# Kernel tuning notes

Measured on AMD Instinct MI355X. Metric: run time of the kernel, lower is better.

Reference implementation:

```python
import jax, jax.numpy as jnp
import numpy as np

N = 10000
E = 160000
EMB = 10
ITERS = 3


def _linear_params(key, fan_in, fan_out):
    kw, kb = jax.random.split(key)
    # xavier-normal-ish init for the weight, small uniform for bias (as torch Linear default scale)
    w = jax.random.normal(kw, (fan_in, fan_out), dtype=jnp.float32) * np.float32(np.sqrt(2.0 / (fan_in + fan_out)))
    b = jax.random.uniform(kb, (fan_out,), dtype=jnp.float32, minval=-0.1, maxval=0.1)
    return w, b


def setup_inputs() -> dict:
    key = jax.random.key(0)
    ks = jax.random.split(key, 10)
    features = jax.random.normal(ks[0], (N,), dtype=jnp.float32)
    weights = jax.random.uniform(ks[1], (E,), dtype=jnp.float32)
    adjacency = jax.random.uniform(ks[2], (N, N), dtype=jnp.float32)
    ws_w, ws_b = _linear_params(ks[3], 1, EMB)          # w_selected
    wnp_w, wnp_b = _linear_params(ks[4], EMB, EMB)      # w_nbpriors
    wnw_w, wnw_b = _linear_params(ks[5], EMB, EMB)      # w_nbweights
    wew_w, wew_b = _linear_params(ks[6], 1, EMB)        # w_nbweights_ew
    wqr_w, wqr_b = _linear_params(ks[7], 2 * EMB, 1)    # w_q_reduc
    wqa_w, wqa_b = _linear_params(ks[8], EMB, EMB)      # w_q_allembed
    wqact_w, wqact_b = _linear_params(ks[9], EMB, EMB)  # w_q_action
    return {
        "features": features, "weights": weights, "adjacency": adjacency,
        "ws_w": ws_w, "ws_b": ws_b,
        "wnp_w": wnp_w, "wnp_b": wnp_b,
        "wnw_w": wnw_w, "wnw_b": wnw_b,
        "wew_w": wew_w, "wew_b": wew_b,
        "wqr_w": wqr_w, "wqr_b": wqr_b,
        "wqa_w": wqa_w, "wqa_b": wqa_b,
        "wqact_w": wqact_w, "wqact_b": wqact_b,
    }


def reference(features, weights, adjacency,
              ws_w, ws_b, wnp_w, wnp_b, wnw_w, wnw_b, wew_w, wew_b,
              wqr_w, wqr_b, wqa_w, wqa_b, wqact_w, wqact_b):
    n = adjacency.shape[0]
    # v_selected = w_selected(features[:, None])  -> (N, EMB)
    v_selected = features[:, None] @ ws_w + ws_b
    # edge weight embedding, summed over edges -> single (EMB,) vector
    edge_emb = jax.nn.relu(weights[:, None] @ wew_w + wew_b)  # (E, EMB)
    v_weights = jnp.sum(edge_emb, axis=0) @ wnw_w + wnw_b     # (EMB,)

    embeddings = jnp.zeros((n, EMB), dtype=features.dtype)
    for _ in range(ITERS):  # small fixed iteration count
        v_priors = (adjacency @ embeddings) @ wnp_w + wnp_b   # (N, EMB)
        embeddings = jax.nn.relu(v_selected + v_weights + v_priors)

    sumembed = jnp.sum(embeddings, axis=0) @ wqa_w + wqa_b    # (EMB,)
    peract = embeddings @ wqact_w + wqact_b                   # (N, EMB)
    q_in = jnp.concatenate([jnp.broadcast_to(sumembed[None, :], (n, EMB)), peract], axis=1)
    q_vals = (q_in @ wqr_w + wqr_b)[:, 0]                     # (N,)
    return q_vals, embeddings
```

## Files before the change

### kernel.cpp

```cpp
#include <hip/hip_runtime.h>

#define N_NODES 10000
#define EMB 10
#define NCHUNK 2500
#define ROWS 4

typedef float f32x4 __attribute__((ext_vector_type(4)));

#define WS_SEDGE 0
#define WS_CBASE 16
#define WS_SSUM  32
#define WS_QVEC  48
#define WS_EMBA  64
#define WS_EMBTA (64 + 100000)
#define WS_EMBB  (64 + 200000)
#define WS_EMBTB (64 + 300000)

__global__ void k_edge_sum(const float* __restrict__ w, int E,
                           const float* __restrict__ wew_w,
                           const float* __restrict__ wew_b,
                           float* __restrict__ sEdge) {
    __shared__ float red[4][EMB];
    float a[EMB], b[EMB], acc[EMB];
#pragma unroll
    for (int j = 0; j < EMB; ++j) { a[j] = wew_w[j]; b[j] = wew_b[j]; acc[j] = 0.f; }
    for (int e = blockIdx.x * blockDim.x + threadIdx.x; e < E; e += gridDim.x * blockDim.x) {
        float we = w[e];
#pragma unroll
        for (int j = 0; j < EMB; ++j) acc[j] += fmaxf(we * a[j] + b[j], 0.f);
    }
#pragma unroll
    for (int m = 1; m < 64; m <<= 1)
#pragma unroll
        for (int j = 0; j < EMB; ++j) acc[j] += __shfl_xor(acc[j], m, 64);
    int wave = threadIdx.x >> 6, lane = threadIdx.x & 63;
    if (lane == 0)
#pragma unroll
        for (int j = 0; j < EMB; ++j) red[wave][j] = acc[j];
    __syncthreads();
    if (threadIdx.x < EMB)
        atomicAdd(&sEdge[threadIdx.x],
                  red[0][threadIdx.x] + red[1][threadIdx.x] + red[2][threadIdx.x] + red[3][threadIdx.x]);
}

__global__ void k_prep1(const float* __restrict__ sEdge, const float* __restrict__ wnw_w,
                        const float* __restrict__ wnw_b, const float* __restrict__ ws_b,
                        float* __restrict__ cbase) {
    int j = threadIdx.x;
    if (j < EMB) {
        float v = wnw_b[j];
        for (int k = 0; k < EMB; ++k) v += sEdge[k] * wnw_w[k * EMB + j];
        cbase[j] = v + ws_b[j];
    }
}

__global__ void k_emb1(const float* __restrict__ f, const float* __restrict__ ws_w,
                       const float* __restrict__ cbase, const float* __restrict__ wnp_b,
                       float* __restrict__ emb, float* __restrict__ embT) {
    int i = blockIdx.x * blockDim.x + threadIdx.x;
    if (i < N_NODES) {
        float fi = f[i];
#pragma unroll
        for (int j = 0; j < EMB; ++j) {
            float v = fmaxf(fi * ws_w[j] + cbase[j] + wnp_b[j], 0.f);
            emb[(size_t)i * EMB + j] = v;
            embT[(size_t)j * N_NODES + i] = v;
        }
    }
}

__global__ __launch_bounds__(256) void k_iter(
    const float* __restrict__ A, const float* __restrict__ embT_in,
    const float* __restrict__ f, const float* __restrict__ ws_w,
    const float* __restrict__ cbase, const float* __restrict__ wnp_w,
    const float* __restrict__ wnp_b,
    float* __restrict__ emb_out, float* __restrict__ embT_out) {
    const int tid  = threadIdx.x;
    const int wave = tid >> 6;
    const int lane = tid & 63;
    const int r0 = blockIdx.x * ROWS;

    float acc[ROWS][EMB] = {};

    const f32x4* A0 = (const f32x4*)(A + (size_t)(r0 + 0) * N_NODES);
    const f32x4* A1 = (const f32x4*)(A + (size_t)(r0 + 1) * N_NODES);
    const f32x4* A2 = (const f32x4*)(A + (size_t)(r0 + 2) * N_NODES);
    const f32x4* A3 = (const f32x4*)(A + (size_t)(r0 + 3) * N_NODES);

#pragma unroll 1
    for (int s = 0; s < 9; ++s) {
        int c = s * 256 + tid;
        f32x4 a0 = __builtin_nontemporal_load(A0 + c);
        f32x4 a1 = __builtin_nontemporal_load(A1 + c);
        f32x4 a2 = __builtin_nontemporal_load(A2 + c);
        f32x4 a3 = __builtin_nontemporal_load(A3 + c);
#pragma unroll
        for (int j = 0; j < EMB; ++j) {
            f32x4 e = ((const f32x4*)(embT_in + (size_t)j * N_NODES))[c];
            acc[0][j] += a0.x * e.x + a0.y * e.y + a0.z * e.z + a0.w * e.w;
            acc[1][j] += a1.x * e.x + a1.y * e.y + a1.z * e.z + a1.w * e.w;
            acc[2][j] += a2.x * e.x + a2.y * e.y + a2.z * e.z + a2.w * e.w;
            acc[3][j] += a3.x * e.x + a3.y * e.y + a3.z * e.z + a3.w * e.w;
        }
    }
    if (tid < NCHUNK - 9 * 256) {
        int c = 9 * 256 + tid;
        f32x4 a0 = __builtin_nontemporal_load(A0 + c);
        f32x4 a1 = __builtin_nontemporal_load(A1 + c);
        f32x4 a2 = __builtin_nontemporal_load(A2 + c);
        f32x4 a3 = __builtin_nontemporal_load(A3 + c);
#pragma unroll
        for (int j = 0; j < EMB; ++j) {
            f32x4 e = ((const f32x4*)(embT_in + (size_t)j * N_NODES))[c];
            acc[0][j] += a0.x * e.x + a0.y * e.y + a0.z * e.z + a0.w * e.w;
            acc[1][j] += a1.x * e.x + a1.y * e.y + a1.z * e.z + a1.w * e.w;
            acc[2][j] += a2.x * e.x + a2.y * e.y + a2.z * e.z + a2.w * e.w;
            acc[3][j] += a3.x * e.x + a3.y * e.y + a3.z * e.z + a3.w * e.w;
        }
    }

#pragma unroll
    for (int m = 1; m < 64; m <<= 1)
#pragma unroll
        for (int r = 0; r < ROWS; ++r)
#pragma unroll
            for (int j = 0; j < EMB; ++j) acc[r][j] += __shfl_xor(acc[r][j], m, 64);

    __shared__ float part[4][ROWS * EMB];
    if (lane == 0)
#pragma unroll
        for (int r = 0; r < ROWS; ++r)
#pragma unroll
            for (int j = 0; j < EMB; ++j) part[wave][r * EMB + j] = acc[r][j];
    __syncthreads();

    if (tid < ROWS * EMB) {
        int r = tid / EMB, j = tid % EMB;
        float v = wnp_b[j];
#pragma unroll
        for (int k = 0; k < EMB; ++k) {
            float yk = part[0][r * EMB + k] + part[1][r * EMB + k] +
                       part[2][r * EMB + k] + part[3][r * EMB + k];
            v += yk * wnp_w[k * EMB + j];
        }
        int i = r0 + r;
        v = fmaxf(f[i] * ws_w[j] + cbase[j] + v, 0.f);
        emb_out[(size_t)i * EMB + j] = v;
        embT_out[(size_t)j * N_NODES + i] = v;
    }
}

__global__ void k_colsum(const float* __restrict__ embT, float* __restrict__ ssum) {
    int j = blockIdx.x % EMB;
    int s = blockIdx.x / EMB;
    float acc = 0.f;
    for (int i = s * blockDim.x + threadIdx.x; i < N_NODES; i += (gridDim.x / EMB) * blockDim.x)
        acc += embT[(size_t)j * N_NODES + i];
#pragma unroll
    for (int m = 1; m < 64; m <<= 1) acc += __shfl_xor(acc, m, 64);
    __shared__ float red[4];
    int wave = threadIdx.x >> 6, lane = threadIdx.x & 63;
    if (lane == 0) red[wave] = acc;
    __syncthreads();
    if (threadIdx.x == 0) atomicAdd(&ssum[j], red[0] + red[1] + red[2] + red[3]);
}

__global__ void k_prep2(const float* __restrict__ ssum, const float* __restrict__ wqa_w,
                        const float* __restrict__ wqa_b, const float* __restrict__ wqr_w,
                        const float* __restrict__ wqr_b, const float* __restrict__ wqact_w,
                        const float* __restrict__ wqact_b,
                        float* __restrict__ qvec, float* __restrict__ qc) {
    int t = threadIdx.x;
    float contrib = 0.f;
    if (t < EMB) {
        float se = wqa_b[t];
        for (int k = 0; k < EMB; ++k) se += ssum[k] * wqa_w[k * EMB + t];
        contrib = se * wqr_w[t] + wqact_b[t] * wqr_w[EMB + t];
        float qv = 0.f;
        for (int j = 0; j < EMB; ++j) qv += wqact_w[t * EMB + j] * wqr_w[EMB + j];
        qvec[t] = qv;
    }
#pragma unroll
    for (int m = 1; m < 64; m <<= 1) contrib += __shfl_xor(contrib, m, 64);
    if (t == 0) qc[0] = contrib + wqr_b[0];
}

__global__ void k_out(const float* __restrict__ emb, const float* __restrict__ qvec,
                      const float* __restrict__ qc, float* __restrict__ out) {
    int i = blockIdx.x * blockDim.x + threadIdx.x;
    if (i < N_NODES) {
        float q = qc[0];
        float row[EMB];
#pragma unroll
        for (int j = 0; j < EMB; ++j) {
            row[j] = emb[(size_t)i * EMB + j];
            q += row[j] * qvec[j];
        }
        out[i] = q;
#pragma unroll
        for (int j = 0; j < EMB; ++j) out[N_NODES + (size_t)i * EMB + j] = row[j];
    }
}

extern "C" void kernel_launch(void* const* d_in, const int* in_sizes, int n_in,
                              void* d_out, int out_size, void* d_ws, size_t ws_size,
                              hipStream_t stream) {
    (void)n_in; (void)out_size; (void)ws_size;
    const float* f      = (const float*)d_in[0];
    const float* w      = (const float*)d_in[1];
    const float* A      = (const float*)d_in[2];
    const float* ws_w   = (const float*)d_in[3];
    const float* ws_b   = (const float*)d_in[4];
    const float* wnp_w  = (const float*)d_in[5];
    const float* wnp_b  = (const float*)d_in[6];
    const float* wnw_w  = (const float*)d_in[7];
    const float* wnw_b  = (const float*)d_in[8];
    const float* wew_w  = (const float*)d_in[9];
    const float* wew_b  = (const float*)d_in[10];
    const float* wqr_w  = (const float*)d_in[11];
    const float* wqr_b  = (const float*)d_in[12];
    const float* wqa_w  = (const float*)d_in[13];
    const float* wqa_b  = (const float*)d_in[14];
    const float* wqact_w = (const float*)d_in[15];
    const float* wqact_b = (const float*)d_in[16];
    float* ws  = (float*)d_ws;
    float* out = (float*)d_out;
    const int E = in_sizes[1];

    hipMemsetAsync(ws, 0, 64 * sizeof(float), stream);
    k_edge_sum<<<256, 256, 0, stream>>>(w, E, wew_w, wew_b, ws + WS_SEDGE);
    k_prep1<<<1, 64, 0, stream>>>(ws + WS_SEDGE, wnw_w, wnw_b, ws_b, ws + WS_CBASE);
    k_emb1<<<(N_NODES + 255) / 256, 256, 0, stream>>>(f, ws_w, ws + WS_CBASE, wnp_b,
                                                      ws + WS_EMBA, ws + WS_EMBTA);
    k_iter<<<N_NODES / ROWS, 256, 0, stream>>>(A, ws + WS_EMBTA, f, ws_w, ws + WS_CBASE,
                                               wnp_w, wnp_b, ws + WS_EMBB, ws + WS_EMBTB);
    k_iter<<<N_NODES / ROWS, 256, 0, stream>>>(A, ws + WS_EMBTB, f, ws_w, ws + WS_CBASE,
                                               wnp_w, wnp_b, ws + WS_EMBA, ws + WS_EMBTA);
    k_colsum<<<80, 256, 0, stream>>>(ws + WS_EMBTA, ws + WS_SSUM);
    k_prep2<<<1, 64, 0, stream>>>(ws + WS_SSUM, wqa_w, wqa_b, wqr_w, wqr_b,
                                  wqact_w, wqact_b, ws + WS_QVEC, ws + WS_QVEC + 10);
    k_out<<<(N_NODES + 255) / 256, 256, 0, stream>>>(ws + WS_EMBA, ws + WS_QVEC,
                                                     ws + WS_QVEC + 10, out);
}
```

Before: 694.4 us.

## Fuse prep/first-embedding/colsum kernels into iteration kernels and reverse block order

```diff
diff --git a/kernel.cpp b/kernel.cpp
--- a/kernel.cpp
+++ b/kernel.cpp
@@ -8,13 +8,8 @@
 typedef float f32x4 __attribute__((ext_vector_type(4)));
 
 #define WS_SEDGE 0
-#define WS_CBASE 16
-#define WS_SSUM  32
-#define WS_QVEC  48
-#define WS_EMBA  64
-#define WS_EMBTA (64 + 100000)
-#define WS_EMBB  (64 + 200000)
-#define WS_EMBTB (64 + 300000)
+#define WS_SSUM  16
+#define WS_EMBT  64
 
 __global__ void k_edge_sum(const float* __restrict__ w, int E,
                            const float* __restrict__ wew_w,
@@ -43,42 +38,33 @@
                   red[0][threadIdx.x] + red[1][threadIdx.x] + red[2][threadIdx.x] + red[3][threadIdx.x]);
 }
 
-__global__ void k_prep1(const float* __restrict__ sEdge, const float* __restrict__ wnw_w,
-                        const float* __restrict__ wnw_b, const float* __restrict__ ws_b,
-                        float* __restrict__ cbase) {
-    int j = threadIdx.x;
-    if (j < EMB) {
-        float v = wnw_b[j];
-        for (int k = 0; k < EMB; ++k) v += sEdge[k] * wnw_w[k * EMB + j];
-        cbase[j] = v + ws_b[j];
-    }
-}
-
-__global__ void k_emb1(const float* __restrict__ f, const float* __restrict__ ws_w,
-                       const float* __restrict__ cbase, const float* __restrict__ wnp_b,
-                       float* __restrict__ emb, float* __restrict__ embT) {
-    int i = blockIdx.x * blockDim.x + threadIdx.x;
-    if (i < N_NODES) {
-        float fi = f[i];
-#pragma unroll
-        for (int j = 0; j < EMB; ++j) {
-            float v = fmaxf(fi * ws_w[j] + cbase[j] + wnp_b[j], 0.f);
-            emb[(size_t)i * EMB + j] = v;
-            embT[(size_t)j * N_NODES + i] = v;
-        }
-    }
-}
-
+template <bool FIRST>
 __global__ __launch_bounds__(256) void k_iter(
     const float* __restrict__ A, const float* __restrict__ embT_in,
     const float* __restrict__ f, const float* __restrict__ ws_w,
-    const float* __restrict__ cbase, const float* __restrict__ wnp_w,
-    const float* __restrict__ wnp_b,
-    float* __restrict__ emb_out, float* __restrict__ embT_out) {
+    const float* __restrict__ ws_b, const float* __restrict__ wnp_w,
+    const float* __restrict__ wnp_b, const float* __restrict__ wnw_w,
+    const float* __restrict__ wnw_b, const float* __restrict__ sEdge,
+    float* __restrict__ embT_out, float* __restrict__ emb_out,
+    float* __restrict__ ssum) {
     const int tid  = threadIdx.x;
     const int wave = tid >> 6;
     const int lane = tid & 63;
-    const int r0 = blockIdx.x * ROWS;
+    const int bid  = FIRST ? blockIdx.x : (gridDim.x - 1 - blockIdx.x);
+    const int r0   = bid * ROWS;
+
+    __shared__ float s_cb2[EMB];
+    if (tid < EMB) {
+        int j = tid;
+        float v = wnw_b[j];
+#pragma unroll
+        for (int k = 0; k < EMB; ++k) v += sEdge[k] * wnw_w[k * EMB + j];
+        s_cb2[j] = v + ws_b[j] + wnp_b[j];
+    }
+    __syncthreads();
+    float cb2[EMB], wsw[EMB];
+#pragma unroll
+    for (int j = 0; j < EMB; ++j) { cb2[j] = s_cb2[j]; wsw[j] = ws_w[j]; }
 
     float acc[ROWS][EMB] = {};
 
@@ -86,38 +72,43 @@
     const f32x4* A1 = (const f32x4*)(A + (size_t)(r0 + 1) * N_NODES);
     const f32x4* A2 = (const f32x4*)(A + (size_t)(r0 + 2) * N_NODES);
     const f32x4* A3 = (const f32x4*)(A + (size_t)(r0 + 3) * N_NODES);
+    const f32x4* F4 = (const f32x4*)f;
+
+#define BODY(c)                                                                     \
+    {                                                                               \
+        f32x4 a0, a1, a2, a3;                                                       \
+        if (FIRST) {                                                                \
+            a0 = A0[c]; a1 = A1[c]; a2 = A2[c]; a3 = A3[c];                         \
+        } else {                                                                    \
+            a0 = __builtin_nontemporal_load(A0 + (c));                              \
+            a1 = __builtin_nontemporal_load(A1 + (c));                              \
+            a2 = __builtin_nontemporal_load(A2 + (c));                              \
+            a3 = __builtin_nontemporal_load(A3 + (c));                              \
+        }                                                                           \
+        f32x4 f4;                                                                   \
+        if (FIRST) f4 = F4[c];                                                      \
+        _Pragma("unroll")                                                           \
+        for (int j = 0; j < EMB; ++j) {                                             \
+            f32x4 e;                                                               \
+            if (FIRST) {                                                            \
+                e.x = fmaxf(f4.x * wsw[j] + cb2[j], 0.f);                           \
+                e.y = fmaxf(f4.y * wsw[j] + cb2[j], 0.f);                           \
+                e.z = fmaxf(f4.z * wsw[j] + cb2[j], 0.f);                           \
+                e.w = fmaxf(f4.w * wsw[j] + cb2[j], 0.f);                           \
+            } else {                                                                \
+                e = ((const f32x4*)(embT_in + (size_t)j * N_NODES))[c];             \
+            }                                                                       \
+            acc[0][j] += a0.x * e.x + a0.y * e.y + a0.z * e.z + a0.w * e.w;         \
+            acc[1][j] += a1.x * e.x + a1.y * e.y + a1.z * e.z + a1.w * e.w;         \
+            acc[2][j] += a2.x * e.x + a2.y * e.y + a2.z * e.z + a2.w * e.w;         \
+            acc[3][j] += a3.x * e.x + a3.y * e.y + a3.z * e.z + a3.w * e.w;         \
+        }                                                                           \
+    }
 
 #pragma unroll 1
-    for (int s = 0; s < 9; ++s) {
-        int c = s * 256 + tid;
-        f32x4 a0 = __builtin_nontemporal_load(A0 + c);
-        f32x4 a1 = __builtin_nontemporal_load(A1 + c);
-        f32x4 a2 = __builtin_nontemporal_load(A2 + c);
-        f32x4 a3 = __builtin_nontemporal_load(A3 + c);
-#pragma unroll
-        for (int j = 0; j < EMB; ++j) {
-            f32x4 e = ((const f32x4*)(embT_in + (size_t)j * N_NODES))[c];
-            acc[0][j] += a0.x * e.x + a0.y * e.y + a0.z * e.z + a0.w * e.w;
-            acc[1][j] += a1.x * e.x + a1.y * e.y + a1.z * e.z + a1.w * e.w;
-            acc[2][j] += a2.x * e.x + a2.y * e.y + a2.z * e.z + a2.w * e.w;
-            acc[3][j] += a3.x * e.x + a3.y * e.y + a3.z * e.z + a3.w * e.w;
-        }
-    }
-    if (tid < NCHUNK - 9 * 256) {
-        int c = 9 * 256 + tid;
-        f32x4 a0 = __builtin_nontemporal_load(A0 + c);
-        f32x4 a1 = __builtin_nontemporal_load(A1 + c);
-        f32x4 a2 = __builtin_nontemporal_load(A2 + c);
-        f32x4 a3 = __builtin_nontemporal_load(A3 + c);
-#pragma unroll
-        for (int j = 0; j < EMB; ++j) {
-            f32x4 e = ((const f32x4*)(embT_in + (size_t)j * N_NODES))[c];
-            acc[0][j] += a0.x * e.x + a0.y * e.y + a0.z * e.z + a0.w * e.w;
-            acc[1][j] += a1.x * e.x + a1.y * e.y + a1.z * e.z + a1.w * e.w;
-            acc[2][j] += a2.x * e.x + a2.y * e.y + a2.z * e.z + a2.w * e.w;
-            acc[3][j] += a3.x * e.x + a3.y * e.y + a3.z * e.z + a3.w * e.w;
-        }
-    }
+    for (int s = 0; s < 9; ++s) { int c = s * 256 + tid; BODY(c) }
+    if (tid < NCHUNK - 9 * 256) { int c = 9 * 256 + tid; BODY(c) }
+#undef BODY
 
 #pragma unroll
     for (int m = 1; m < 64; m <<= 1)
@@ -127,6 +118,7 @@
             for (int j = 0; j < EMB; ++j) acc[r][j] += __shfl_xor(acc[r][j], m, 64);
 
     __shared__ float part[4][ROWS * EMB];
+    __shared__ float colp[ROWS * EMB];
     if (lane == 0)
 #pragma unroll
         for (int r = 0; r < ROWS; ++r)
@@ -136,7 +128,7 @@
 
     if (tid < ROWS * EMB) {
         int r = tid / EMB, j = tid % EMB;
-        float v = wnp_b[j];
+        float v = 0.f;
 #pragma unroll
         for (int k = 0; k < EMB; ++k) {
             float yk = part[0][r * EMB + k] + part[1][r * EMB + k] +
@@ -144,61 +136,52 @@
             v += yk * wnp_w[k * EMB + j];
         }
         int i = r0 + r;
-        v = fmaxf(f[i] * ws_w[j] + cbase[j] + v, 0.f);
-        emb_out[(size_t)i * EMB + j] = v;
-        embT_out[(size_t)j * N_NODES + i] = v;
-    }
-}
-
-__global__ void k_colsum(const float* __restrict__ embT, float* __restrict__ ssum) {
-    int j = blockIdx.x % EMB;
-    int s = blockIdx.x / EMB;
-    float acc = 0.f;
-    for (int i = s * blockDim.x + threadIdx.x; i < N_NODES; i += (gridDim.x / EMB) * blockDim.x)
-        acc += embT[(size_t)j * N_NODES + i];
-#pragma unroll
-    for (int m = 1; m < 64; m <<= 1) acc += __shfl_xor(acc, m, 64);
-    __shared__ float red[4];
-    int wave = threadIdx.x >> 6, lane = threadIdx.x & 63;
-    if (lane == 0) red[wave] = acc;
-    __syncthreads();
-    if (threadIdx.x == 0) atomicAdd(&ssum[j], red[0] + red[1] + red[2] + red[3]);
-}
-
-__global__ void k_prep2(const float* __restrict__ ssum, const float* __restrict__ wqa_w,
-                        const float* __restrict__ wqa_b, const float* __restrict__ wqr_w,
-                        const float* __restrict__ wqr_b, const float* __restrict__ wqact_w,
-                        const float* __restrict__ wqact_b,
-                        float* __restrict__ qvec, float* __restrict__ qc) {
+        v = fmaxf(f[i] * wsw[j] + cb2[j] + v, 0.f);
+        if (FIRST) {
+            embT_out[(size_t)j * N_NODES + i] = v;
+        } else {
+            emb_out[(size_t)i * EMB + j] = v;
+            colp[tid] = v;
+        }
+    }
+    if (!FIRST) {
+        __syncthreads();
+        if (tid < EMB)
+            atomicAdd(&ssum[tid],
+                      colp[tid] + colp[EMB + tid] + colp[2 * EMB + tid] + colp[3 * EMB + tid]);
+    }
+}
+
+__global__ void k_out(const float* __restrict__ embRM, const float* __restrict__ ssum,
+                      const float* __restrict__ wqa_w, const float* __restrict__ wqa_b,
+                      const float* __restrict__ wqr_w, const float* __restrict__ wqr_b,
+                      const float* __restrict__ wqact_w, const float* __restrict__ wqact_b,
+                      float* __restrict__ q_out) {
+    __shared__ float s_qvec[EMB];
+    __shared__ float s_qc;
     int t = threadIdx.x;
-    float contrib = 0.f;
+    if (t == 0) {
+        float qc = wqr_b[0];
+        for (int tt = 0; tt < EMB; ++tt) {
+            float se = wqa_b[tt];
+            for (int k = 0; k < EMB; ++k) se += ssum[k] * wqa_w[k * EMB + tt];
+            qc += se * wqr_w[tt] + wqact_b[tt] * wqr_w[EMB + tt];
+        }
+        s_qc = qc;
+    }
     if (t < EMB) {
-        float se = wqa_b[t];
-        for (int k = 0; k < EMB; ++k) se += ssum[k] * wqa_w[k * EMB + t];
-        contrib = se * wqr_w[t] + wqact_b[t] * wqr_w[EMB + t];
         float qv = 0.f;
+#pragma unroll
         for (int j = 0; j < EMB; ++j) qv += wqact_w[t * EMB + j] * wqr_w[EMB + j];
-        qvec[t] = qv;
-    }
-#pragma unroll
-    for (int m = 1; m < 64; m <<= 1) contrib += __shfl_xor(contrib, m, 64);
-    if (t == 0) qc[0] = contrib + wqr_b[0];
-}
-
-__global__ void k_out(const float* __restrict__ emb, const float* __restrict__ qvec,
-                      const float* __restrict__ qc, float* __restrict__ out) {
-    int i = blockIdx.x * blockDim.x + threadIdx.x;
+        s_qvec[t] = qv;
+    }
+    __syncthreads();
+    int i = blockIdx.x * blockDim.x + t;
     if (i < N_NODES) {
-        float q = qc[0];
-        float row[EMB];
-#pragma unroll
-        for (int j = 0; j < EMB; ++j) {
-            row[j] = emb[(size_t)i * EMB + j];
-            q += row[j] * qvec[j];
-        }
-        out[i] = q;
-#pragma unroll
-        for (int j = 0; j < EMB; ++j) out[N_NODES + (size_t)i * EMB + j] = row[j];
+        float q = s_qc;
+#pragma unroll
+        for (int j = 0; j < EMB; ++j) q += embRM[(size_t)i * EMB + j] * s_qvec[j];
+        q_out[i] = q;
     }
 }
 
@@ -227,18 +210,17 @@
     float* out = (float*)d_out;
     const int E = in_sizes[1];
 
+    float* outEmb = out + N_NODES;
+
     hipMemsetAsync(ws, 0, 64 * sizeof(float), stream);
     k_edge_sum<<<256, 256, 0, stream>>>(w, E, wew_w, wew_b, ws + WS_SEDGE);
-    k_prep1<<<1, 64, 0, stream>>>(ws + WS_SEDGE, wnw_w, wnw_b, ws_b, ws + WS_CBASE);
-    k_emb1<<<(N_NODES + 255) / 256, 256, 0, stream>>>(f, ws_w, ws + WS_CBASE, wnp_b,
-                                                      ws + WS_EMBA, ws + WS_EMBTA);
-    k_iter<<<N_NODES / ROWS, 256, 0, stream>>>(A, ws + WS_EMBTA, f, ws_w, ws + WS_CBASE,
-                                               wnp_w, wnp_b, ws + WS_EMBB, ws + WS_EMBTB);
-    k_iter<<<N_NODES / ROWS, 256, 0, stream>>>(A, ws + WS_EMBTB, f, ws_w, ws + WS_CBASE,
-                                               wnp_w, wnp_b, ws + WS_EMBA, ws + WS_EMBTA);
-    k_colsum<<<80, 256, 0, stream>>>(ws + WS_EMBTA, ws + WS_SSUM);
-    k_prep2<<<1, 64, 0, stream>>>(ws + WS_SSUM, wqa_w, wqa_b, wqr_w, wqr_b,
-                                  wqact_w, wqact_b, ws + WS_QVEC, ws + WS_QVEC + 10);
-    k_out<<<(N_NODES + 255) / 256, 256, 0, stream>>>(ws + WS_EMBA, ws + WS_QVEC,
-                                                     ws + WS_QVEC + 10, out);
-}
+    k_iter<true><<<N_NODES / ROWS, 256, 0, stream>>>(
+        A, nullptr, f, ws_w, ws_b, wnp_w, wnp_b, wnw_w, wnw_b, ws + WS_SEDGE,
+        ws + WS_EMBT, nullptr, nullptr);
+    k_iter<false><<<N_NODES / ROWS, 256, 0, stream>>>(
+        A, ws + WS_EMBT, f, ws_w, ws_b, wnp_w, wnp_b, wnw_w, wnw_b, ws + WS_SEDGE,
+        nullptr, outEmb, ws + WS_SSUM);
+    k_out<<<(N_NODES + 255) / 256, 256, 0, stream>>>(outEmb, ws + WS_SSUM,
+                                                     wqa_w, wqa_b, wqr_w, wqr_b,
+                                                     wqact_w, wqact_b, out);
+}
```

Result: faster. 680.5 us (-2.0%).
